# Kernel optimization log

Hardware: AMD Instinct MI355X
Metric: run time of the kernel (lower is better)

The kernel has to match this reference:

```python
import jax, jax.numpy as jnp
import numpy as np

DIM = 384
HEADS = 12
HD = DIM // HEADS  # 32
WIN = 16
N = WIN * WIN      # 256
B = 256            # num_windows * batch
K = 5              # dwc kernel size
EPS = 1e-6


def setup_inputs() -> dict:
    key = jax.random.key(0)
    ks = jax.random.split(key, 8)
    u = lambda k, shape, fan_in: jax.random.uniform(
        k, shape, jnp.float32, -1.0 / np.sqrt(fan_in), 1.0 / np.sqrt(fan_in))
    return {
        "x": jax.random.normal(ks[0], (B, N, DIM), jnp.float32),
        # nn.Linear(dim, 3*dim): weight [3C, C], bias [3C]
        "qkv_w": u(ks[1], (3 * DIM, DIM), DIM),
        "qkv_b": u(ks[2], (3 * DIM,), DIM),
        # nn.Parameter initialized to zeros
        "pos_enc": jnp.zeros((1, N, DIM), jnp.float32),
        # depthwise Conv2d(HD, HD, K, groups=HD): weight [HD, 1, K, K]
        "dwc_w": u(ks[3], (HD, 1, K, K), K * K),
        "dwc_b": u(ks[4], (HD,), K * K),
        "proj_w": u(ks[5], (DIM, DIM), DIM),
        "proj_b": u(ks[6], (DIM,), DIM),
    }


def reference(x, qkv_w, qkv_b, pos_enc, dwc_w, dwc_b, proj_w, proj_b):
    Bsz, Nn, C = x.shape
    qkv = x @ qkv_w.T + qkv_b                     # [B, N, 3C]
    q, k, v = jnp.split(qkv, 3, axis=-1)          # each [B, N, C]
    k = k + pos_enc
    q = jax.nn.relu(q)
    k = jax.nn.relu(k)

    def to_heads(t):  # 'b n (h c) -> (b h) n c'
        return t.reshape(Bsz, Nn, HEADS, HD).transpose(0, 2, 1, 3).reshape(Bsz * HEADS, Nn, HD)

    q, k, v = to_heads(q), to_heads(k), to_heads(v)
    # explicit fp32 (autocast disabled block in original)
    qf = q.astype(jnp.float32)
    kf = k.astype(jnp.float32)
    vf = v.astype(jnp.float32)

    z = 1.0 / (jnp.einsum('bic,bc->bi', qf, kf.sum(axis=1)) + EPS)  # [BH, N]

    i = j = Nn
    c = d = HD
    if i * j * (c + d) > c * d * (i + j):  # kv-first (true for N=256, HD=32)
        kv = jnp.einsum('bjc,bjd->bcd', kf, vf)            # [BH, c, d]
        out = jnp.einsum('bic,bcd,bi->bid', qf, kv, z)     # [BH, N, d]
    else:
        qk = jnp.einsum('bic,bjc->bij', qf, kf)
        out = jnp.einsum('bij,bjd,bi->bid', qk, vf, z)

    # depthwise conv on v: 'b (w h) c -> b c w h'
    num = int(Nn ** 0.5)
    fm = vf.reshape(Bsz * HEADS, num, num, HD).transpose(0, 3, 1, 2)  # NCHW
    fm = jax.lax.conv_general_dilated(
        fm, dwc_w, window_strides=(1, 1),
        padding=[(K // 2, K // 2), (K // 2, K // 2)],
        dimension_numbers=('NCHW', 'OIHW', 'NCHW'),
        feature_group_count=HD)
    fm = fm + dwc_b[None, :, None, None]
    fm = fm.transpose(0, 2, 3, 1).reshape(Bsz * HEADS, Nn, HD)  # 'b c w h -> b (w h) c'

    out = out + fm
    # '(b h) n c -> b n (h c)'
    out = out.reshape(Bsz, HEADS, Nn, HD).transpose(0, 2, 1, 3).reshape(Bsz, Nn, C)
    return out @ proj_w.T + proj_b
```

## Files before the change

kernel.cpp:

```cpp
#include <hip/hip_runtime.h>
#include <stdint.h>
#include <stddef.h>


typedef _Float16 f16;
typedef __attribute__((ext_vector_type(4))) _Float16 f16x4;
typedef __attribute__((ext_vector_type(8))) _Float16 f16x8;
typedef __attribute__((ext_vector_type(4))) float floatx4;

#define DEV __device__ __forceinline__

DEV void async16(const void* g, void* l) {
  __builtin_amdgcn_global_load_lds(
      (const __attribute__((address_space(1))) void*)g,
      (__attribute__((address_space(3))) void*)l,
      16, 0, 0);
}

DEV floatx4 mfma16(f16x8 a, f16x8 b, floatx4 c) {
  return __builtin_amdgcn_mfma_f32_16x16x32_f16(a, b, c, 0, 0, 0);
}

DEV f16x4 cvt4(float4 v) {
  f16x4 h;
  h[0] = (f16)v.x; h[1] = (f16)v.y; h[2] = (f16)v.z; h[3] = (f16)v.w;
  return h;
}

__global__ __launch_bounds__(256) void cvt_kernel(
    const float* __restrict__ src, f16* __restrict__ dst, int n4) {
  const int stride = gridDim.x * 256;
  for (int i = blockIdx.x * 256 + threadIdx.x; i < n4; i += stride) {
    float4 v = ((const float4*)src)[i];
    ((f16x4*)dst)[i] = cvt4(v);
  }
}

__global__ __launch_bounds__(256) void qkv_kernel(
    const f16* __restrict__ A, const f16* __restrict__ W,
    const float* __restrict__ bias, const float* __restrict__ pos,
    f16* __restrict__ q_ws, f16* __restrict__ kT_ws, f16* __restrict__ vT_ws) {
  __shared__ __align__(16) f16 Af[128 * 64];
  __shared__ __align__(16) f16 Wf[128 * 64];
  const int tid = threadIdx.x;
  const int lane = tid & 63, wave = tid >> 6;
  const int quad = lane >> 4, lr = lane & 15;
  const int wm = wave >> 1, wn = wave & 1;
  const int bx = blockIdx.x;
  const int ga = bx / 72, rem = bx - ga * 72;
  const int nblk = rem >> 3, gc = rem & 7;
  const int m0 = (ga * 8 + gc) * 128, n0 = nblk * 128;
  const int rl = lane >> 3;
  const int lcol = (lane & 7) ^ rl;

  floatx4 acc[4][4] = {};

  const f16* ap[4];
  const f16* wp[4];
#pragma unroll
  for (int t2 = 0; t2 < 4; ++t2) {
    const int row = (wave * 4 + t2) * 8 + rl;
    ap[t2] = A + (size_t)(m0 + row) * 384 + lcol * 8;
    wp[t2] = W + (size_t)(n0 + row) * 384 + lcol * 8;
  }

  for (int kt = 0; kt < 6; ++kt) {
    __syncthreads();
#pragma unroll
    for (int t2 = 0; t2 < 4; ++t2) {
      const int ch = wave * 4 + t2;
      async16(ap[t2] + kt * 64, (char*)Af + ch * 1024);
      async16(wp[t2] + kt * 64, (char*)Wf + ch * 1024);
    }
    __syncthreads();
#pragma unroll
    for (int s = 0; s < 2; ++s) {
      const int pc = ((quad + s * 4) ^ (lr & 7)) * 16;
      f16x8 af[4], wf[4];
#pragma unroll
      for (int mt = 0; mt < 4; ++mt)
        af[mt] = *(const f16x8*)((const char*)Af +
                                 (wm * 64 + mt * 16 + lr) * 128 + pc);
#pragma unroll
      for (int nt = 0; nt < 4; ++nt)
        wf[nt] = *(const f16x8*)((const char*)Wf +
                                 (wn * 64 + nt * 16 + lr) * 128 + pc);
#pragma unroll
      for (int mt = 0; mt < 4; ++mt)
#pragma unroll
        for (int nt = 0; nt < 4; ++nt)
          acc[mt][nt] = mfma16(af[mt], wf[nt], acc[mt][nt]);
    }
  }

  float bv[4];
#pragma unroll
  for (int nt = 0; nt < 4; ++nt)
    bv[nt] = bias[n0 + wn * 64 + nt * 16 + lr];

  const int cls = nblk / 3;
  const int cbase = (nblk - cls * 3) * 128;
  if (cls == 0) {
#pragma unroll
    for (int mt = 0; mt < 4; ++mt) {
#pragma unroll
      for (int r = 0; r < 4; ++r) {
        const int m = m0 + wm * 64 + mt * 16 + quad * 4 + r;
        const int bwin = m >> 8, t = m & 255;
#pragma unroll
        for (int nt = 0; nt < 4; ++nt) {
          const int c = cbase + wn * 64 + nt * 16 + lr;
          const int h = c >> 5, hd = c & 31;
          const float val = fmaxf(acc[mt][nt][r] + bv[nt], 0.f);
          q_ws[(size_t)(bwin * 12 + h) * 8192 + t * 32 + hd] = (f16)val;
        }
      }
    }
  } else {
#pragma unroll
    for (int mt = 0; mt < 4; ++mt) {
      const int mb = m0 + wm * 64 + mt * 16 + quad * 4;
      const int bwin = mb >> 8, t0 = mb & 255;
#pragma unroll
      for (int nt = 0; nt < 4; ++nt) {
        const int c = cbase + wn * 64 + nt * 16 + lr;
        const int h = c >> 5, hd = c & 31;
        f16x4 pk;
        if (cls == 1) {
#pragma unroll
          for (int r = 0; r < 4; ++r)
            pk[r] = (f16)fmaxf(acc[mt][nt][r] + bv[nt] + pos[(t0 + r) * 384 + c], 0.f);
          *(f16x4*)(kT_ws + (size_t)(bwin * 12 + h) * 8192 + hd * 256 + t0) = pk;
        } else {
#pragma unroll
          for (int r = 0; r < 4; ++r)
            pk[r] = (f16)(acc[mt][nt][r] + bv[nt]);
          *(f16x4*)(vT_ws + (size_t)(bwin * 12 + h) * 8192 + hd * 256 + t0) = pk;
        }
      }
    }
  }
}

__global__ __launch_bounds__(256) void attn_kernel(
    const f16* __restrict__ q_ws, const f16* __restrict__ kT_ws,
    const f16* __restrict__ vT_ws, const float* __restrict__ dwc_w,
    const float* __restrict__ dwc_b, f16* __restrict__ y_ws) {
  __shared__ __align__(16) char khb[16640];
  __shared__ __align__(16) char vhb[16640];
  __shared__ __align__(16) float pkv[4 * 32 * 36];
  __shared__ float psum[8 * 32];
  __shared__ float ksum[32];
  __shared__ float zbuf[256];
  __shared__ __align__(16) f16 kvT[32 * 40];

  const int tid = threadIdx.x;
  const int lane = tid & 63, wave = tid >> 6;
  const int quad = lane >> 4, lr = lane & 15;
  const int bh = blockIdx.x;
  const size_t base = (size_t)bh * 8192;

#pragma unroll
  for (int t2 = 0; t2 < 4; ++t2) {
    const int is = wave * 4 + t2;
    async16(kT_ws + base + is * 512 + lane * 8, khb + is * 1040);
    async16(vT_ws + base + is * 512 + lane * 8, vhb + is * 1040);
  }
  __syncthreads();

  {
    const int c = tid & 31, seg = tid >> 5;
    const char* kr = khb + (c >> 1) * 1040 + (c & 1) * 512;
    float s = 0.f;
#pragma unroll
    for (int j8 = 0; j8 < 32; j8 += 8) {
      f16x8 a = *(const f16x8*)(kr + (seg * 32 + j8) * 2);
#pragma unroll
      for (int j = 0; j < 8; ++j) s += (float)a[j];
    }
    psum[seg * 32 + c] = s;
  }
  {
    floatx4 kacc[2][2] = {};
#pragma unroll
    for (int ss = 0; ss < 2; ++ss) {
      const int s = wave * 2 + ss;
      f16x8 ka[2], vb[2];
#pragma unroll
      for (int m2 = 0; m2 < 2; ++m2) {
        const int c = m2 * 16 + lr;
        const size_t off =
            (size_t)(c >> 1) * 1040 + (c & 1) * 512 + (s * 32 + quad * 8) * 2;
        ka[m2] = *(const f16x8*)(khb + off);
        vb[m2] = *(const f16x8*)(vhb + off);
      }
#pragma unroll
      for (int m2 = 0; m2 < 2; ++m2)
#pragma unroll
        for (int n2 = 0; n2 < 2; ++n2)
          kacc[m2][n2] = mfma16(ka[m2], vb[n2], kacc[m2][n2]);
    }
#pragma unroll
    for (int m2 = 0; m2 < 2; ++m2)
#pragma unroll
      for (int n2 = 0; n2 < 2; ++n2)
#pragma unroll
        for (int r = 0; r < 4; ++r)
          pkv[(wave * 32 + m2 * 16 + quad * 4 + r) * 36 + n2 * 16 + lr] =
              kacc[m2][n2][r];
  }
  __syncthreads();

  if (tid < 32) {
    float s = 0.f;
#pragma unroll
    for (int seg = 0; seg < 8; ++seg) s += psum[seg * 32 + tid];
    ksum[tid] = s;
  }
  {
    const int c = tid >> 3, d0 = (tid & 7) * 4;
#pragma unroll
    for (int dd = 0; dd < 4; ++dd) {
      const int d = d0 + dd;
      float s = pkv[(0 * 32 + c) * 36 + d] + pkv[(1 * 32 + c) * 36 + d] +
                pkv[(2 * 32 + c) * 36 + d] + pkv[(3 * 32 + c) * 36 + d];
      kvT[d * 40 + c] = (f16)s;
    }
  }
  {
    uint32_t* fmu = (uint32_t*)khb;
    const int cg = tid & 15, xr = tid >> 4, c0 = cg * 2;
    float a0[16], a1[16];
    const float b0v = dwc_b[c0], b1v = dwc_b[c0 + 1];
#pragma unroll
    for (int yy = 0; yy < 16; ++yy) { a0[yy] = b0v; a1[yy] = b1v; }
    const char* v0 = vhb + cg * 1040;
#pragma unroll
    for (int dx = 0; dx < 5; ++dx) {
      const int xx = xr + dx - 2;
      if (xx < 0 || xx > 15) continue;
      float r0[16], r1[16];
      f16x8 h0 = *(const f16x8*)(v0 + xx * 32);
      f16x8 h1 = *(const f16x8*)(v0 + xx * 32 + 16);
      f16x8 h2 = *(const f16x8*)(v0 + 512 + xx * 32);
      f16x8 h3 = *(const f16x8*)(v0 + 512 + xx * 32 + 16);
#pragma unroll
      for (int j = 0; j < 8; ++j) {
        r0[j] = (float)h0[j]; r0[8 + j] = (float)h1[j];
        r1[j] = (float)h2[j]; r1[8 + j] = (float)h3[j];
      }
#pragma unroll
      for (int dy = 0; dy < 5; ++dy) {
        const float w0 = dwc_w[c0 * 25 + dx * 5 + dy];
        const float w1 = dwc_w[(c0 + 1) * 25 + dx * 5 + dy];
#pragma unroll
        for (int yy = 0; yy < 16; ++yy) {
          const int ys = yy + dy - 2;
          if (ys >= 0 && ys < 16) {
            a0[yy] += w0 * r0[ys];
            a1[yy] += w1 * r1[ys];
          }
        }
      }
    }
#pragma unroll
    for (int yy = 0; yy < 16; ++yy) {
      const uint32_t lo = (uint32_t)__builtin_bit_cast(uint16_t, (f16)a0[yy]);
      const uint32_t hi = (uint32_t)__builtin_bit_cast(uint16_t, (f16)a1[yy]);
      fmu[(xr * 16 + yy) * 16 + cg] = lo | (hi << 16);
    }
  }
  __syncthreads();

  {
    const f16* qrow = q_ws + base + (size_t)tid * 32;
    float dot = 0.f;
#pragma unroll
    for (int c8 = 0; c8 < 32; c8 += 8) {
      f16x8 qq = *(const f16x8*)(qrow + c8);
#pragma unroll
      for (int j = 0; j < 8; ++j) dot += (float)qq[j] * ksum[c8 + j];
    }
    zbuf[tid] = 1.f / (dot + 1e-6f);
  }
  {
    floatx4 oacc[4][2] = {};
    f16x8 qa[4], kb[2];
#pragma unroll
    for (int mm = 0; mm < 4; ++mm)
      qa[mm] = *(const f16x8*)(q_ws + base +
                               (size_t)(wave * 64 + mm * 16 + lr) * 32 + quad * 8);
#pragma unroll
    for (int nt = 0; nt < 2; ++nt)
      kb[nt] = *(const f16x8*)(kvT + (nt * 16 + lr) * 40 + quad * 8);
#pragma unroll
    for (int mm = 0; mm < 4; ++mm)
#pragma unroll
      for (int nt = 0; nt < 2; ++nt)
        oacc[mm][nt] = mfma16(qa[mm], kb[nt], oacc[mm][nt]);

    const f16* fmb = (const f16*)khb;
#pragma unroll
    for (int mm = 0; mm < 4; ++mm) {
#pragma unroll
      for (int r = 0; r < 4; ++r) {
        const int i = wave * 64 + mm * 16 + quad * 4 + r;
        const float zi = zbuf[i];
#pragma unroll
        for (int nt = 0; nt < 2; ++nt) {
          const int d = nt * 16 + lr;
          const float val = oacc[mm][nt][r] * zi + (float)fmb[i * 32 + d];
          y_ws[base + (size_t)i * 32 + d] = (f16)val;
        }
      }
    }
  }
}

__global__ __launch_bounds__(256) void proj_kernel(
    const f16* __restrict__ Y, const f16* __restrict__ Wh,
    const float* __restrict__ bias, float* __restrict__ out) {
  __shared__ __align__(16) f16 Af[128 * 64];
  __shared__ __align__(16) f16 Wf[128 * 64];
  const int tid = threadIdx.x;
  const int lane = tid & 63, wave = tid >> 6;
  const int quad = lane >> 4, lr = lane & 15;
  const int wm = wave >> 1, wn = wave & 1;
  const int bx = blockIdx.x;
  const int ga = bx / 24, rem = bx - ga * 24;
  const int nblk = rem >> 3, gc = rem & 7;
  const int m0 = (ga * 8 + gc) * 128, n0 = nblk * 128;
  const int bwin = m0 >> 8, tbase = m0 & 255;
  const int rl = lane >> 3;
  const int lcol = (lane & 7) ^ rl;

  floatx4 acc[4][4] = {};

  const f16* ap[4];
  const f16* wp[4];
#pragma unroll
  for (int t2 = 0; t2 < 4; ++t2) {
    const int rowl = (wave * 4 + t2) * 8 + rl;
    ap[t2] = Y + (size_t)(bwin * 12 + (lcol >> 2)) * 8192 +
             (size_t)(tbase + rowl) * 32 + (lcol & 3) * 8;
    wp[t2] = Wh + (size_t)(n0 + rowl) * 384 + lcol * 8;
  }

  for (int kt = 0; kt < 6; ++kt) {
    __syncthreads();
#pragma unroll
    for (int t2 = 0; t2 < 4; ++t2) {
      const int ch = wave * 4 + t2;
      async16(ap[t2] + (size_t)kt * 16384, (char*)Af + ch * 1024);
      async16(wp[t2] + kt * 64, (char*)Wf + ch * 1024);
    }
    __syncthreads();
#pragma unroll
    for (int s = 0; s < 2; ++s) {
      const int pc = ((quad + s * 4) ^ (lr & 7)) * 16;
      f16x8 af[4], wf[4];
#pragma unroll
      for (int mt = 0; mt < 4; ++mt)
        af[mt] = *(const f16x8*)((const char*)Af +
                                 (wm * 64 + mt * 16 + lr) * 128 + pc);
#pragma unroll
      for (int nt = 0; nt < 4; ++nt)
        wf[nt] = *(const f16x8*)((const char*)Wf +
                                 (wn * 64 + nt * 16 + lr) * 128 + pc);
#pragma unroll
      for (int mt = 0; mt < 4; ++mt)
#pragma unroll
        for (int nt = 0; nt < 4; ++nt)
          acc[mt][nt] = mfma16(af[mt], wf[nt], acc[mt][nt]);
    }
  }

  float bv[4];
#pragma unroll
  for (int nt = 0; nt < 4; ++nt)
    bv[nt] = bias[n0 + wn * 64 + nt * 16 + lr];
#pragma unroll
  for (int mt = 0; mt < 4; ++mt)
#pragma unroll
    for (int r = 0; r < 4; ++r) {
      const int m = m0 + wm * 64 + mt * 16 + quad * 4 + r;
#pragma unroll
      for (int nt = 0; nt < 4; ++nt) {
        const int n = n0 + wn * 64 + nt * 16 + lr;
        out[(size_t)m * 384 + n] = acc[mt][nt][r] + bv[nt];
      }
    }
}

extern "C" void kernel_launch(void* const* d_in, const int* in_sizes, int n_in,
                              void* d_out, int out_size, void* d_ws, size_t ws_size,
                              hipStream_t stream) {
  const float* x = (const float*)d_in[0];
  const float* qkv_w = (const float*)d_in[1];
  const float* qkv_b = (const float*)d_in[2];
  const float* pos = (const float*)d_in[3];
  const float* dwc_w = (const float*)d_in[4];
  const float* dwc_b = (const float*)d_in[5];
  const float* proj_w = (const float*)d_in[6];
  const float* proj_b = (const float*)d_in[7];
  float* out = (float*)d_out;

  const size_t WS_NEEDED = 150994944;
  if (ws_size < WS_NEEDED) return;

  char* ws = (char*)d_ws;
  f16* q_ws = (f16*)(ws);
  f16* kT_ws = (f16*)(ws + 50331648);
  f16* vT_ws = (f16*)(ws + 100663296);

  f16* xh = (f16*)d_out;
  f16* qwh = (f16*)((char*)d_out + 50331648);
  f16* pwh = (f16*)(ws + 50331648);

  cvt_kernel<<<2048, 256, 0, stream>>>(x, xh, 6291456);
  cvt_kernel<<<432, 256, 0, stream>>>(qkv_w, qwh, 110592);
  qkv_kernel<<<4608, 256, 0, stream>>>(xh, qwh, qkv_b, pos,
                                       q_ws, kT_ws, vT_ws);
  attn_kernel<<<3072, 256, 0, stream>>>(q_ws, kT_ws, vT_ws,
                                        dwc_w, dwc_b, q_ws );
  cvt_kernel<<<144, 256, 0, stream>>>(proj_w, pwh, 36864);
  proj_kernel<<<1536, 256, 0, stream>>>(q_ws, pwh, proj_b, out);
}
```

Before: 367.0 us.

## Make attention waves independent with redundant per-wave KV and no block barriers

The attention kernel no longer stages K and V into shared memory with async loads. Each wave now reads K^T and V^T straight from global memory and computes the full 32x32 KV product and the K column sums in its own registers. Those sums are reduced with cross-lane shuffles into per-wave buffers, and the depthwise-conv and output phases are remapped so each wave only touches its own 64 rows. This removes all block-wide __syncthreads and the cross-wave partial-sum reductions. In exchange, K and V are read four times per block (presumably hitting cache) and the KV MFMA work is repeated in every wave.

```diff
diff --git a/kernel.cpp b/kernel.cpp
--- a/kernel.cpp
+++ b/kernel.cpp
@@ -146,53 +146,33 @@
     const f16* __restrict__ q_ws, const f16* __restrict__ kT_ws,
     const f16* __restrict__ vT_ws, const float* __restrict__ dwc_w,
     const float* __restrict__ dwc_b, f16* __restrict__ y_ws) {
-  __shared__ __align__(16) char khb[16640];
-  __shared__ __align__(16) char vhb[16640];
-  __shared__ __align__(16) float pkv[4 * 32 * 36];
-  __shared__ float psum[8 * 32];
-  __shared__ float ksum[32];
+  __shared__ __align__(16) f16 fmbuf[256 * 32];
+  __shared__ __align__(16) f16 kvT[4][32 * 40];
+  __shared__ float ksum[4][32];
   __shared__ float zbuf[256];
-  __shared__ __align__(16) f16 kvT[32 * 40];
 
   const int tid = threadIdx.x;
   const int lane = tid & 63, wave = tid >> 6;
   const int quad = lane >> 4, lr = lane & 15;
-  const int bh = blockIdx.x;
-  const size_t base = (size_t)bh * 8192;
-
-#pragma unroll
-  for (int t2 = 0; t2 < 4; ++t2) {
-    const int is = wave * 4 + t2;
-    async16(kT_ws + base + is * 512 + lane * 8, khb + is * 1040);
-    async16(vT_ws + base + is * 512 + lane * 8, vhb + is * 1040);
-  }
-  __syncthreads();
-
-  {
-    const int c = tid & 31, seg = tid >> 5;
-    const char* kr = khb + (c >> 1) * 1040 + (c & 1) * 512;
-    float s = 0.f;
-#pragma unroll
-    for (int j8 = 0; j8 < 32; j8 += 8) {
-      f16x8 a = *(const f16x8*)(kr + (seg * 32 + j8) * 2);
-#pragma unroll
-      for (int j = 0; j < 8; ++j) s += (float)a[j];
-    }
-    psum[seg * 32 + c] = s;
-  }
+  const size_t base = (size_t)blockIdx.x * 8192;
+
   {
     floatx4 kacc[2][2] = {};
-#pragma unroll
-    for (int ss = 0; ss < 2; ++ss) {
-      const int s = wave * 2 + ss;
+    float ks0 = 0.f, ks1 = 0.f;
+#pragma unroll
+    for (int s = 0; s < 8; ++s) {
       f16x8 ka[2], vb[2];
 #pragma unroll
       for (int m2 = 0; m2 < 2; ++m2) {
-        const int c = m2 * 16 + lr;
         const size_t off =
-            (size_t)(c >> 1) * 1040 + (c & 1) * 512 + (s * 32 + quad * 8) * 2;
-        ka[m2] = *(const f16x8*)(khb + off);
-        vb[m2] = *(const f16x8*)(vhb + off);
+            base + (size_t)(m2 * 16 + lr) * 256 + s * 32 + quad * 8;
+        ka[m2] = *(const f16x8*)(kT_ws + off);
+        vb[m2] = *(const f16x8*)(vT_ws + off);
+      }
+#pragma unroll
+      for (int j = 0; j < 8; ++j) {
+        ks0 += (float)ka[0][j];
+        ks1 += (float)ka[1][j];
       }
 #pragma unroll
       for (int m2 = 0; m2 < 2; ++m2)
@@ -200,50 +180,51 @@
         for (int n2 = 0; n2 < 2; ++n2)
           kacc[m2][n2] = mfma16(ka[m2], vb[n2], kacc[m2][n2]);
     }
+    ks0 += __shfl_xor(ks0, 16); ks0 += __shfl_xor(ks0, 32);
+    ks1 += __shfl_xor(ks1, 16); ks1 += __shfl_xor(ks1, 32);
+    if (quad == 0) {
+      ksum[wave][lr] = ks0;
+      ksum[wave][16 + lr] = ks1;
+    }
 #pragma unroll
     for (int m2 = 0; m2 < 2; ++m2)
 #pragma unroll
       for (int n2 = 0; n2 < 2; ++n2)
 #pragma unroll
         for (int r = 0; r < 4; ++r)
-          pkv[(wave * 32 + m2 * 16 + quad * 4 + r) * 36 + n2 * 16 + lr] =
-              kacc[m2][n2][r];
-  }
-  __syncthreads();
-
-  if (tid < 32) {
-    float s = 0.f;
-#pragma unroll
-    for (int seg = 0; seg < 8; ++seg) s += psum[seg * 32 + tid];
-    ksum[tid] = s;
-  }
+          kvT[wave][(n2 * 16 + lr) * 40 + m2 * 16 + quad * 4 + r] =
+              (f16)kacc[m2][n2][r];
+  }
+
   {
-    const int c = tid >> 3, d0 = (tid & 7) * 4;
-#pragma unroll
-    for (int dd = 0; dd < 4; ++dd) {
-      const int d = d0 + dd;
-      float s = pkv[(0 * 32 + c) * 36 + d] + pkv[(1 * 32 + c) * 36 + d] +
-                pkv[(2 * 32 + c) * 36 + d] + pkv[(3 * 32 + c) * 36 + d];
-      kvT[d * 40 + c] = (f16)s;
-    }
-  }
+    const f16* qrow = q_ws + base + (size_t)(wave * 64 + lane) * 32;
+    float dot = 0.f;
+#pragma unroll
+    for (int c8 = 0; c8 < 32; c8 += 8) {
+      f16x8 qq = *(const f16x8*)(qrow + c8);
+#pragma unroll
+      for (int j = 0; j < 8; ++j) dot += (float)qq[j] * ksum[wave][c8 + j];
+    }
+    zbuf[wave * 64 + lane] = 1.f / (dot + 1e-6f);
+  }
+
   {
-    uint32_t* fmu = (uint32_t*)khb;
-    const int cg = tid & 15, xr = tid >> 4, c0 = cg * 2;
+    uint32_t* fmu = (uint32_t*)fmbuf;
+    const int cg = lr, xr = wave * 4 + quad, c0 = cg * 2;
     float a0[16], a1[16];
     const float b0v = dwc_b[c0], b1v = dwc_b[c0 + 1];
 #pragma unroll
     for (int yy = 0; yy < 16; ++yy) { a0[yy] = b0v; a1[yy] = b1v; }
-    const char* v0 = vhb + cg * 1040;
+    const f16* v0 = vT_ws + base + c0 * 256;
 #pragma unroll
     for (int dx = 0; dx < 5; ++dx) {
       const int xx = xr + dx - 2;
       if (xx < 0 || xx > 15) continue;
       float r0[16], r1[16];
-      f16x8 h0 = *(const f16x8*)(v0 + xx * 32);
-      f16x8 h1 = *(const f16x8*)(v0 + xx * 32 + 16);
-      f16x8 h2 = *(const f16x8*)(v0 + 512 + xx * 32);
-      f16x8 h3 = *(const f16x8*)(v0 + 512 + xx * 32 + 16);
+      f16x8 h0 = *(const f16x8*)(v0 + xx * 16);
+      f16x8 h1 = *(const f16x8*)(v0 + xx * 16 + 8);
+      f16x8 h2 = *(const f16x8*)(v0 + 256 + xx * 16);
+      f16x8 h3 = *(const f16x8*)(v0 + 256 + xx * 16 + 8);
 #pragma unroll
       for (int j = 0; j < 8; ++j) {
         r0[j] = (float)h0[j]; r0[8 + j] = (float)h1[j];
@@ -270,19 +251,7 @@
       fmu[(xr * 16 + yy) * 16 + cg] = lo | (hi << 16);
     }
   }
-  __syncthreads();
-
-  {
-    const f16* qrow = q_ws + base + (size_t)tid * 32;
-    float dot = 0.f;
-#pragma unroll
-    for (int c8 = 0; c8 < 32; c8 += 8) {
-      f16x8 qq = *(const f16x8*)(qrow + c8);
-#pragma unroll
-      for (int j = 0; j < 8; ++j) dot += (float)qq[j] * ksum[c8 + j];
-    }
-    zbuf[tid] = 1.f / (dot + 1e-6f);
-  }
+
   {
     floatx4 oacc[4][2] = {};
     f16x8 qa[4], kb[2];
@@ -292,14 +261,13 @@
                                (size_t)(wave * 64 + mm * 16 + lr) * 32 + quad * 8);
 #pragma unroll
     for (int nt = 0; nt < 2; ++nt)
-      kb[nt] = *(const f16x8*)(kvT + (nt * 16 + lr) * 40 + quad * 8);
+      kb[nt] = *(const f16x8*)(kvT[wave] + (nt * 16 + lr) * 40 + quad * 8);
 #pragma unroll
     for (int mm = 0; mm < 4; ++mm)
 #pragma unroll
       for (int nt = 0; nt < 2; ++nt)
         oacc[mm][nt] = mfma16(qa[mm], kb[nt], oacc[mm][nt]);
 
-    const f16* fmb = (const f16*)khb;
 #pragma unroll
     for (int mm = 0; mm < 4; ++mm) {
 #pragma unroll
@@ -309,7 +277,7 @@
 #pragma unroll
         for (int nt = 0; nt < 2; ++nt) {
           const int d = nt * 16 + lr;
-          const float val = oacc[mm][nt][r] * zi + (float)fmb[i * 32 + d];
+          const float val = oacc[mm][nt][r] * zi + (float)fmbuf[i * 32 + d];
           y_ws[base + (size_t)i * 32 + d] = (f16)val;
         }
       }
```

New measurement: 404.0 us. +10.1%, slower.

## Split KV tiles across waves and drop a barrier in attention kernel

Applied to the files above, without the earlier changes.

Each wave now computes one full 16x16 tile of K^T V over all 256 tokens and writes it straight to kvT as f16, which removes the pkv partial-sum buffer and its reduction pass. Each wave keeps its own copy of ksum, and z is computed from the q fragments already held in registers using lane shuffles, so the extra global q load and one __syncthreads are gone. The depthwise-conv thread mapping is remapped so each wave writes rows aligned with its own output rows. The intent is to cut LDS traffic, shared memory use and barriers. The cost is that correctness now depends on per-wave data locality, because zbuf and the conv output are read without a block-wide barrier.

```diff
diff --git a/kernel.cpp b/kernel.cpp
--- a/kernel.cpp
+++ b/kernel.cpp
@@ -148,17 +148,15 @@
     const float* __restrict__ dwc_b, f16* __restrict__ y_ws) {
   __shared__ __align__(16) char khb[16640];
   __shared__ __align__(16) char vhb[16640];
-  __shared__ __align__(16) float pkv[4 * 32 * 36];
   __shared__ float psum[8 * 32];
-  __shared__ float ksum[32];
+  __shared__ float ksum[4][32];
   __shared__ float zbuf[256];
   __shared__ __align__(16) f16 kvT[32 * 40];
 
   const int tid = threadIdx.x;
   const int lane = tid & 63, wave = tid >> 6;
   const int quad = lane >> 4, lr = lane & 15;
-  const int bh = blockIdx.x;
-  const size_t base = (size_t)bh * 8192;
+  const size_t base = (size_t)blockIdx.x * 8192;
 
 #pragma unroll
   for (int t2 = 0; t2 < 4; ++t2) {
@@ -181,55 +179,34 @@
     psum[seg * 32 + c] = s;
   }
   {
-    floatx4 kacc[2][2] = {};
-#pragma unroll
-    for (int ss = 0; ss < 2; ++ss) {
-      const int s = wave * 2 + ss;
-      f16x8 ka[2], vb[2];
-#pragma unroll
-      for (int m2 = 0; m2 < 2; ++m2) {
-        const int c = m2 * 16 + lr;
-        const size_t off =
-            (size_t)(c >> 1) * 1040 + (c & 1) * 512 + (s * 32 + quad * 8) * 2;
-        ka[m2] = *(const f16x8*)(khb + off);
-        vb[m2] = *(const f16x8*)(vhb + off);
-      }
-#pragma unroll
-      for (int m2 = 0; m2 < 2; ++m2)
-#pragma unroll
-        for (int n2 = 0; n2 < 2; ++n2)
-          kacc[m2][n2] = mfma16(ka[m2], vb[n2], kacc[m2][n2]);
-    }
-#pragma unroll
-    for (int m2 = 0; m2 < 2; ++m2)
-#pragma unroll
-      for (int n2 = 0; n2 < 2; ++n2)
-#pragma unroll
-        for (int r = 0; r < 4; ++r)
-          pkv[(wave * 32 + m2 * 16 + quad * 4 + r) * 36 + n2 * 16 + lr] =
-              kacc[m2][n2][r];
+    const int m2 = wave & 1, n2 = wave >> 1;
+    const int ck = m2 * 16 + lr, cv = n2 * 16 + lr;
+    const char* krow = khb + (ck >> 1) * 1040 + (ck & 1) * 512;
+    const char* vrow = vhb + (cv >> 1) * 1040 + (cv & 1) * 512;
+    floatx4 kacc = {};
+#pragma unroll
+    for (int s = 0; s < 8; ++s) {
+      f16x8 ka = *(const f16x8*)(krow + (s * 32 + quad * 8) * 2);
+      f16x8 vb = *(const f16x8*)(vrow + (s * 32 + quad * 8) * 2);
+      kacc = mfma16(ka, vb, kacc);
+    }
+    f16x4 kk;
+#pragma unroll
+    for (int r = 0; r < 4; ++r) kk[r] = (f16)kacc[r];
+    *(f16x4*)(kvT + (n2 * 16 + lr) * 40 + m2 * 16 + quad * 4) = kk;
   }
   __syncthreads();
 
-  if (tid < 32) {
+  if (lane < 32) {
     float s = 0.f;
 #pragma unroll
-    for (int seg = 0; seg < 8; ++seg) s += psum[seg * 32 + tid];
-    ksum[tid] = s;
-  }
-  {
-    const int c = tid >> 3, d0 = (tid & 7) * 4;
-#pragma unroll
-    for (int dd = 0; dd < 4; ++dd) {
-      const int d = d0 + dd;
-      float s = pkv[(0 * 32 + c) * 36 + d] + pkv[(1 * 32 + c) * 36 + d] +
-                pkv[(2 * 32 + c) * 36 + d] + pkv[(3 * 32 + c) * 36 + d];
-      kvT[d * 40 + c] = (f16)s;
-    }
-  }
+    for (int seg = 0; seg < 8; ++seg) s += psum[seg * 32 + lane];
+    ksum[wave][lane] = s;
+  }
+
   {
     uint32_t* fmu = (uint32_t*)khb;
-    const int cg = tid & 15, xr = tid >> 4, c0 = cg * 2;
+    const int cg = lr, xr = wave * 4 + quad, c0 = cg * 2;
     float a0[16], a1[16];
     const float b0v = dwc_b[c0], b1v = dwc_b[c0 + 1];
 #pragma unroll
@@ -270,26 +247,28 @@
       fmu[(xr * 16 + yy) * 16 + cg] = lo | (hi << 16);
     }
   }
-  __syncthreads();
 
   {
-    const f16* qrow = q_ws + base + (size_t)tid * 32;
-    float dot = 0.f;
-#pragma unroll
-    for (int c8 = 0; c8 < 32; c8 += 8) {
-      f16x8 qq = *(const f16x8*)(qrow + c8);
-#pragma unroll
-      for (int j = 0; j < 8; ++j) dot += (float)qq[j] * ksum[c8 + j];
-    }
-    zbuf[tid] = 1.f / (dot + 1e-6f);
-  }
-  {
-    floatx4 oacc[4][2] = {};
     f16x8 qa[4], kb[2];
 #pragma unroll
     for (int mm = 0; mm < 4; ++mm)
       qa[mm] = *(const f16x8*)(q_ws + base +
                                (size_t)(wave * 64 + mm * 16 + lr) * 32 + quad * 8);
+
+    float ksv[8];
+#pragma unroll
+    for (int j = 0; j < 8; ++j) ksv[j] = ksum[wave][quad * 8 + j];
+#pragma unroll
+    for (int mm = 0; mm < 4; ++mm) {
+      float dot = 0.f;
+#pragma unroll
+      for (int j = 0; j < 8; ++j) dot += (float)qa[mm][j] * ksv[j];
+      dot += __shfl_xor(dot, 16);
+      dot += __shfl_xor(dot, 32);
+      if (quad == 0) zbuf[wave * 64 + mm * 16 + lr] = 1.f / (dot + 1e-6f);
+    }
+
+    floatx4 oacc[4][2] = {};
 #pragma unroll
     for (int nt = 0; nt < 2; ++nt)
       kb[nt] = *(const f16x8*)(kvT + (nt * 16 + lr) * 40 + quad * 8);
```

Result: faster. 351.0 us (-4.4%).
